# Kernel optimization log

Measured on AMD Instinct MI355X. Metric: run time of the kernel, lower is better.

## Reference

```python
import jax, jax.numpy as jnp
from jax import lax
import numpy as np

B, A, F, S, NA = 16, 5, 4, 45, 6


def _xavier(key, shape, fan_in, fan_out):
    lim = float(np.sqrt(6.0 / (fan_in + fan_out)))
    return jax.random.uniform(key, shape, jnp.float32, -lim, lim)


def setup_inputs() -> dict:
    key = jax.random.key(0)
    ks = jax.random.split(key, 16)
    x = jax.random.uniform(ks[0], (B, A, F, S, S, S), jnp.float32, 0.0, 255.0)
    p = lambda: jnp.full((1,), 0.25, jnp.float32)  # PReLU init
    return {
        "x": x,
        "conv0_w": _xavier(ks[1], (32, F, 5, 5, 5), F * 125, 32 * 125),
        "conv0_b": jnp.zeros((32,), jnp.float32),
        "prelu0": p(),
        "conv1_w": _xavier(ks[2], (32, 32, 5, 5, 5), 32 * 125, 32 * 125),
        "conv1_b": jnp.zeros((32,), jnp.float32),
        "prelu1": p(),
        "conv2_w": _xavier(ks[3], (64, 32, 4, 4, 4), 32 * 64, 64 * 64),
        "conv2_b": jnp.zeros((64,), jnp.float32),
        "prelu2": p(),
        "conv3_w": _xavier(ks[4], (64, 64, 3, 3, 3), 64 * 27, 64 * 27),
        "conv3_b": jnp.zeros((64,), jnp.float32),
        "prelu3": p(),
        "fc1_w": _xavier(ks[5], (A, 256, 1024), 1024, 256),
        "fc1_b": jnp.zeros((A, 256), jnp.float32),
        "prelu4": p(),
        "fc2_w": _xavier(ks[6], (A, 128, 512), 512, 128),
        "fc2_b": jnp.zeros((A, 128), jnp.float32),
        "prelu5": p(),
        "fc3_w": _xavier(ks[7], (A, NA, 256), 256, NA),
        "fc3_b": jnp.zeros((A, NA), jnp.float32),
    }


def _conv3d(x, w, b, pad):
    y = lax.conv_general_dilated(
        x, w, window_strides=(1, 1, 1), padding=[(pad, pad)] * 3,
        dimension_numbers=("NCDHW", "OIDHW", "NCDHW"))
    return y + b[None, :, None, None, None]


def _maxpool2(x):
    return lax.reduce_window(x, -jnp.inf, lax.max,
                             (1, 1, 2, 2, 2), (1, 1, 2, 2, 2), "VALID")


def _prelu(x, a):
    return jnp.where(x >= 0, x, a * x)


def _comm_fc(feat, w, b):
    # feat: [B,A,D]; w: [A,O,2D]; b: [A,O]. concat(feat, mean-over-agents) -> per-agent linear
    comm = jnp.mean(feat, axis=1, keepdims=True)
    cat = jnp.concatenate([feat, jnp.broadcast_to(comm, feat.shape)], axis=-1)
    return jnp.einsum("bai,aoi->bao", cat, w) + b[None]


def reference(x, conv0_w, conv0_b, prelu0, conv1_w, conv1_b, prelu1,
              conv2_w, conv2_b, prelu2, conv3_w, conv3_b, prelu3,
              fc1_w, fc1_b, prelu4, fc2_w, fc2_b, prelu5, fc3_w, fc3_b):
    b, a = x.shape[0], x.shape[1]
    # fold agents into batch: conv stack is shared across agents
    h = x.reshape((b * a,) + x.shape[2:]) / 255.0
    h = _maxpool2(_prelu(_conv3d(h, conv0_w, conv0_b, 1), prelu0))
    h = _maxpool2(_prelu(_conv3d(h, conv1_w, conv1_b, 1), prelu1))
    h = _maxpool2(_prelu(_conv3d(h, conv2_w, conv2_b, 1), prelu2))
    h = _prelu(_conv3d(h, conv3_w, conv3_b, 0), prelu3)
    feat = h.reshape(b, a, -1)  # [B, A, 512]
    feat = _prelu(_comm_fc(feat, fc1_w, fc1_b), prelu4)   # [B, A, 256]
    feat = _prelu(_comm_fc(feat, fc2_w, fc2_b), prelu5)   # [B, A, 128]
    return _comm_fc(feat, fc3_w, fc3_b)                   # [B, A, NA]
```

## Files before the change

### kernel.cpp

```cpp
#include <hip/hip_runtime.h>


typedef __attribute__((ext_vector_type(8)))  _Float16 f16x8;
typedef __attribute__((ext_vector_type(8), aligned(8))) _Float16 f16x8u;
typedef __attribute__((ext_vector_type(4)))  float f32x4;

__device__ __forceinline__ ushort f2h(float f) {
    union { _Float16 h; ushort u; } v;
    v.h = (_Float16)f;
    return v.u;
}
__device__ __forceinline__ float h2f(ushort h) {
    union { ushort u; _Float16 h; } v; v.u = h;
    return (float)v.h;
}

#define MFMA16(A, B, C) __builtin_amdgcn_mfma_f32_16x16x32_f16(A, B, C, 0, 0, 0)

__global__ void pad_input_kernel(const float* __restrict__ x,
                                 ushort* __restrict__ hi)
{
    int t = blockIdx.x * 256 + threadIdx.x;
    const int TOT = 80 * 45 * 45 * 45;
    if (t >= TOT) return;
    int xi = t % 45, r = t / 45;
    int y = r % 45; r /= 45;
    int z = r % 45; int n = r / 45;
    int ib = ((n * 4) * 91125) + z * 2025 + y * 45 + xi;
    int ob = (((n * 47 + z + 1) * 47 + y + 1) * 48 + xi + 1) * 4;
    ushort h4[4];
    #pragma unroll
    for (int ic = 0; ic < 4; ++ic) {
        float v = x[ib + ic * 91125] * (1.f / 255.f);
        h4[ic] = f2h(v);
    }
    *(ushort4*)(hi + ob) = *(ushort4*)h4;
}

__global__ void pack_w0(const float* __restrict__ w, ushort* __restrict__ Bp,
                        int4* __restrict__ Dt)
{
    int t = blockIdx.x * 256 + threadIdx.x;
    if (t < 19 * 2 * 64 * 8) {
        int j = t & 7, l = (t >> 3) & 63, ot = (t >> 9) & 1, s = t >> 10;
        int oc = ot * 16 + (l & 15);
        int k = 32 * s + ((l >> 4) << 3) + j;
        float v = 0.f;
        if (k < 600) {
            int ic = k & 3, t6 = k >> 2;
            int kx = t6 % 6, q = t6 / 6, ky = q % 5, kz = q / 5;
            if (kx < 5) v = w[(oc * 4 + ic) * 125 + kz * 25 + ky * 5 + kx];
        }
        Bp[t] = f2h(v);
    }
    if (t < 19) {
        int dd[4];
        #pragma unroll
        for (int q = 0; q < 4; ++q) {
            int k = 32 * t + 8 * q;
            if (k < 600) {
                int t6 = k >> 2;
                int kx = t6 % 6, qq = t6 / 6;
                dd[q] = (((qq / 5) * 47 + (qq % 5)) * 48 + kx) * 4;
            } else dd[q] = 0;
        }
        int4 d; d.x = dd[0]; d.y = dd[1]; d.z = dd[2]; d.w = dd[3];
        Dt[t] = d;
    }
}

__global__ void pack_w1(const float* __restrict__ w, ushort* __restrict__ Bp,
                        int* __restrict__ Dt)
{
    int t = blockIdx.x * 256 + threadIdx.x;
    if (t < 126 * 2 * 64 * 8) {
        int j = t & 7, l = (t >> 3) & 63, ot = (t >> 9) & 1, s = t >> 10;
        int oc = ot * 16 + (l & 15);
        int ic = ((l >> 4) << 3) + j;
        Bp[t] = (s < 125) ? f2h(w[(oc * 32 + ic) * 125 + s]) : (ushort)0;
    }
    if (t < 126) {
        if (t < 125) {
            int kz = t / 25, ky = (t / 5) % 5, kx = t % 5;
            Dt[t] = ((kz * 23 + ky) * 24 + kx) * 32;
        } else Dt[t] = 0;
    }
}

__global__ void pack_w2(const float* __restrict__ w,
                        ushort* __restrict__ Bh, ushort* __restrict__ Bl,
                        int* __restrict__ Dt)
{
    int t = blockIdx.x * 256 + threadIdx.x;
    if (t < 64 * 4 * 64 * 8) {
        int j = t & 7, l = (t >> 3) & 63, nt = (t >> 9) & 3, s = t >> 11;
        int oc = nt * 16 + (l & 15);
        int ic = ((l >> 4) << 3) + j;
        int kz = s >> 4, ky = (s >> 2) & 3, kx = s & 3;
        float v = w[(oc * 32 + ic) * 64 + kz * 16 + ky * 4 + kx];
        ushort h = f2h(v);
        Bh[t] = h;
        Bl[t] = f2h(v - h2f(h));
    }
    if (t < 64) {
        int kz = t >> 4, ky = (t >> 2) & 3, kx = t & 3;
        Dt[t] = ((kz * 11 + ky) * 12 + kx) * 32;
    }
}

__global__ __launch_bounds__(256, 2)
void conv0_mfma(const ushort* __restrict__ hi0,
                const ushort* __restrict__ Bp, const int4* __restrict__ Dt,
                const float* __restrict__ bias, const float* __restrict__ slope,
                ushort* __restrict__ hi1)
{
    const int n   = blockIdx.z;
    const int pz  = blockIdx.x / 11, pyg = blockIdx.x % 11;
    const int tid = threadIdx.x, lane = tid & 63, w = tid >> 6;
    const int dz  = w >> 1, pyl = w & 1;
    const int py  = 2 * pyg + pyl;
    const int l15 = lane & 15, q = lane >> 4;

    __shared__ float pool[2][2][21][32];
    __shared__ __align__(16) ushort Bl[19 * 2 * 64 * 8];

    {
        const uint4* src = (const uint4*)Bp;
        uint4* dst = (uint4*)Bl;
        for (int i = tid; i < 2432; i += 256) dst[i] = src[i];
    }

    const int z0 = 2 * pz + dz;
    const int y0 = 2 * py;
    const float sl = slope[0];

    int ab[3];
    #pragma unroll
    for (int xt = 0; xt < 3; ++xt) {
        int x = xt * 16 + l15;
        int xr = x > 41 ? 41 : x;
        ab[xt] = (((n * 47 + z0) * 47 + y0) * 48 + xr) * 4;
    }

    f32x4 acc[2][3][2] = {};
    const f16x8* BL = (const f16x8*)Bl;

    f16x8 avd[2][3][2];

    auto LOADS = [&](int s, int j) {
        int4 dd = Dt[s];
        int delta = q == 0 ? dd.x : q == 1 ? dd.y : q == 2 ? dd.z : dd.w;
        #pragma unroll
        for (int xt = 0; xt < 3; ++xt) {
            int vo = ab[xt] + delta;
            avd[j][xt][0] = *(const f16x8u*)(hi0 + vo);
            avd[j][xt][1] = *(const f16x8u*)(hi0 + vo + 192);
        }
    };
    auto COMP = [&](int s, int j) {
        f16x8 b0 = BL[(2 * s) * 64 + lane];
        f16x8 b1 = BL[(2 * s + 1) * 64 + lane];
        #pragma unroll
        for (int xt = 0; xt < 3; ++xt)
            #pragma unroll
            for (int dy = 0; dy < 2; ++dy) {
                acc[dy][xt][0] = MFMA16(avd[j][xt][dy], b0, acc[dy][xt][0]);
                acc[dy][xt][1] = MFMA16(avd[j][xt][dy], b1, acc[dy][xt][1]);
            }
    };

    __syncthreads();

    LOADS(0, 0); LOADS(1, 1);
    for (int s = 0; s < 16; s += 2) {
        COMP(s, 0);     LOADS(s + 2, 0);
        COMP(s + 1, 1); LOADS(s + 3, 1);
    }
    COMP(16, 0); LOADS(18, 0);
    COMP(17, 1);
    COMP(18, 0);

    #pragma unroll
    for (int xt = 0; xt < 3; ++xt)
        #pragma unroll
        for (int ot = 0; ot < 2; ++ot) {
            float m0 = fmaxf(acc[0][xt][ot][0], acc[1][xt][ot][0]);
            float m1 = fmaxf(acc[0][xt][ot][1], acc[1][xt][ot][1]);
            float m2 = fmaxf(acc[0][xt][ot][2], acc[1][xt][ot][2]);
            float m3 = fmaxf(acc[0][xt][ot][3], acc[1][xt][ot][3]);
            int pxe = xt * 8 + 2 * q, pxo = pxe + 1;
            if (pxe < 21) pool[dz][pyl][pxe][ot * 16 + l15] = fmaxf(m0, m1);
            if (pxo < 21) pool[dz][pyl][pxo][ot * 16 + l15] = fmaxf(m2, m3);
        }
    __syncthreads();

    for (int t2 = tid; t2 < 1344; t2 += 256) {
        int oc = t2 & 31, r = t2 >> 5;
        int px = r % 21, pyl2 = r / 21;
        int py2 = 2 * pyg + pyl2;
        if (py2 > 20) continue;
        float v = fmaxf(pool[0][pyl2][px][oc], pool[1][pyl2][px][oc]);
        v += bias[oc];
        v = (v >= 0.f) ? v : sl * v;
        int o = (((n * 23 + pz + 1) * 23 + py2 + 1) * 24 + px + 1) * 32 + oc;
        hi1[o] = f2h(v);
    }
}

__global__ __launch_bounds__(256)
void conv1_mfma(const ushort* __restrict__ hi1,
                const ushort* __restrict__ Bp, const int* __restrict__ Dt,
                const float* __restrict__ bias, const float* __restrict__ slope,
                ushort* __restrict__ P2h, ushort* __restrict__ P2l)
{
    const int n   = blockIdx.z;
    const int pz  = blockIdx.x / 3, pyg = blockIdx.x % 3;
    const int tid = threadIdx.x, lane = tid & 63, w = tid >> 6;
    const int dz = w >> 1, dy = w & 1;
    const int q = lane >> 4, l15 = lane & 15;

    __shared__ float pool[4][27][32];
    const int z0 = 2 * pz + dz;

    int ab[4];
    #pragma unroll
    for (int t = 0; t < 4; ++t) {
        int flat = t * 16 + l15;
        if (flat > 53) flat = 53;
        int pyl = flat / 18, x = flat - pyl * 18;
        int y0 = 2 * (pyg * 3 + pyl) + dy;
        ab[t] = ((((n * 23 + z0) * 23 + y0) * 24 + x) << 5) + q * 8;
    }

    f32x4 acc[4][2] = {};
    const f16x8* Bv = (const f16x8*)Bp;

    f16x8 ahv[3][4], b0v[3], b1v[3];

    auto LOADS = [&](int s, int j) {
        int off = Dt[s];
        b0v[j] = Bv[(2 * s) * 64 + lane];
        b1v[j] = Bv[(2 * s + 1) * 64 + lane];
        #pragma unroll
        for (int t = 0; t < 4; ++t)
            ahv[j][t] = *(const f16x8*)(hi1 + ab[t] + off);
    };
    auto COMP = [&](int j) {
        #pragma unroll
        for (int t = 0; t < 4; ++t) {
            acc[t][0] = MFMA16(ahv[j][t], b0v[j], acc[t][0]);
            acc[t][1] = MFMA16(ahv[j][t], b1v[j], acc[t][1]);
        }
    };

    LOADS(0, 0); LOADS(1, 1);
    for (int s = 0; s < 123; s += 3) {
        LOADS(s + 2, 2); COMP(0);
        LOADS(s + 3, 0); COMP(1);
        LOADS(s + 4, 1); COMP(2);
    }
    LOADS(125, 2);
    COMP(0); COMP(1); COMP(2);

    #pragma unroll
    for (int t = 0; t < 4; ++t) {
        int p0 = t * 8 + q * 2;
        float e0 = fmaxf(acc[t][0][0], acc[t][0][1]);
        float o0 = fmaxf(acc[t][0][2], acc[t][0][3]);
        float e1 = fmaxf(acc[t][1][0], acc[t][1][1]);
        float o1 = fmaxf(acc[t][1][2], acc[t][1][3]);
        if (p0 < 27)     { pool[w][p0][l15] = e0;     pool[w][p0][16 + l15] = e1; }
        if (p0 + 1 < 27) { pool[w][p0 + 1][l15] = o0; pool[w][p0 + 1][16 + l15] = o1; }
    }
    __syncthreads();

    for (int t2 = tid; t2 < 864; t2 += 256) {
        int oc = t2 & 31, pr = t2 >> 5;
        int pyl = pr / 9, px = pr % 9;
        float v = fmaxf(fmaxf(pool[0][pr][oc], pool[1][pr][oc]),
                        fmaxf(pool[2][pr][oc], pool[3][pr][oc]));
        v += bias[oc];
        float s0 = slope[0];
        v = (v >= 0.f) ? v : s0 * v;
        int py = pyg * 3 + pyl;
        int o = (((n * 11 + pz + 1) * 11 + py + 1) * 12 + px + 1) * 32 + oc;
        ushort h = f2h(v);
        P2h[o] = h;
        P2l[o] = f2h(v - h2f(h));
    }
}

__global__ __launch_bounds__(256)
void conv2_mfma(const ushort* __restrict__ P2h, const ushort* __restrict__ P2l,
                const ushort* __restrict__ Bph, const ushort* __restrict__ Bpl,
                const int* __restrict__ Dt,
                const float* __restrict__ bias, const float* __restrict__ slope,
                float* __restrict__ P3)
{
    const int n  = blockIdx.x >> 2, zq = blockIdx.x & 3;
    const int tid = threadIdx.x, lane = tid & 63, w = tid >> 6;
    const int q = lane >> 4, l15 = lane & 15;

    __shared__ float pool[2][2][4][4][64];

    const int ozl = w >> 1, oyp0 = 2 * (w & 1);
    const int oz  = zq * 2 + ozl;
    const int myA = l15 >> 3, mxA = l15 & 7;

    int ab[2];
    ab[0] = (((n * 11 + oz) * 11 + oyp0 * 2 + myA) * 12 + mxA) * 32 + q * 8;
    ab[1] = ab[0] + 2 * 12 * 32;

    f32x4 acc[2][4] = {};
    const f16x8* BH = (const f16x8*)Bph;
    const f16x8* BL = (const f16x8*)Bpl;

    f16x8 ahv[2][2], alv[2][2], bhv[2][4], blv[2][4];

    auto LOADS = [&](int s, int j) {
        int d = Dt[s];
        #pragma unroll
        for (int t = 0; t < 2; ++t) {
            ahv[j][t] = *(const f16x8u*)(P2h + ab[t] + d);
            alv[j][t] = *(const f16x8u*)(P2l + ab[t] + d);
        }
        #pragma unroll
        for (int nt = 0; nt < 4; ++nt) {
            bhv[j][nt] = BH[(s * 4 + nt) * 64 + lane];
            blv[j][nt] = BL[(s * 4 + nt) * 64 + lane];
        }
    };
    auto COMP = [&](int j) {
        #pragma unroll
        for (int t = 0; t < 2; ++t)
            #pragma unroll
            for (int nt = 0; nt < 4; ++nt) {
                acc[t][nt] = MFMA16(ahv[j][t], bhv[j][nt], acc[t][nt]);
                acc[t][nt] = MFMA16(alv[j][t], bhv[j][nt], acc[t][nt]);
                acc[t][nt] = MFMA16(ahv[j][t], blv[j][nt], acc[t][nt]);
            }
    };

    LOADS(0, 0); LOADS(1, 1);
    for (int s = 0; s < 62; s += 2) {
        COMP(0); LOADS(s + 2, 0);
        COMP(1); LOADS(s + 3, 1);
    }
    COMP(0); COMP(1);

    const int myD = q >> 1, pxe = (q & 1) * 2;
    #pragma unroll
    for (int t = 0; t < 2; ++t) {
        int py = oyp0 + t;
        #pragma unroll
        for (int nt = 0; nt < 4; ++nt) {
            int oc = nt * 16 + l15;
            pool[myD][ozl][py][pxe][oc]     = fmaxf(acc[t][nt][0], acc[t][nt][1]);
            pool[myD][ozl][py][pxe + 1][oc] = fmaxf(acc[t][nt][2], acc[t][nt][3]);
        }
    }
    __syncthreads();

    for (int t2 = tid; t2 < 1024; t2 += 256) {
        int oc = t2 & 63, r = t2 >> 6;
        int py = r >> 2, px = r & 3;
        float v = fmaxf(fmaxf(pool[0][0][py][px][oc], pool[0][1][py][px][oc]),
                        fmaxf(pool[1][0][py][px][oc], pool[1][1][py][px][oc]));
        v += bias[oc];
        float a = slope[0];
        v = (v >= 0.f) ? v : a * v;
        P3[((long)n * 64 + oc) * 64 + zq * 16 + py * 4 + px] = v;
    }
}

__global__ void conv3_kernel(const float* __restrict__ in,
                             const float* __restrict__ w,
                             const float* __restrict__ bias,
                             const float* __restrict__ slope,
                             float* __restrict__ out)
{
    int idx = blockIdx.x * blockDim.x + threadIdx.x;
    const int TOTAL = 80 * 64 * 8;
    if (idx >= TOTAL) return;
    int p  = idx & 7;
    int oc = (idx >> 3) & 63;
    int n  = idx >> 9;
    int ox = p & 1, oy = (p >> 1) & 1, oz = p >> 2;

    const float* inb = in + (long)n * 64 * 64;
    const float* wb  = w + (long)oc * 64 * 27;

    float acc = 0.f;
    for (int ic = 0; ic < 64; ++ic) {
        const float* inc = inb + ic * 64;
        const float* wc  = wb + ic * 27;
        #pragma unroll
        for (int kz = 0; kz < 3; ++kz)
            #pragma unroll
            for (int ky = 0; ky < 3; ++ky)
                #pragma unroll
                for (int kx = 0; kx < 3; ++kx)
                    acc += wc[(kz * 3 + ky) * 3 + kx] *
                           inc[((oz + kz) * 4 + (oy + ky)) * 4 + (ox + kx)];
    }
    float v = acc + bias[oc];
    float a = slope[0];
    v = (v >= 0.f) ? v : a * v;
    out[idx] = v;
}

template<int D, int O, bool PRELU_ON>
__global__ void comm_fc_kernel(const float* __restrict__ feat,
                               const float* __restrict__ w,
                               const float* __restrict__ bias,
                               const float* __restrict__ slope,
                               float* __restrict__ out)
{
    const int a = blockIdx.x;
    const int b = blockIdx.y;

    __shared__ __align__(16) float cat[2 * D];
    for (int i = threadIdx.x; i < D; i += blockDim.x) {
        float m = 0.f;
        #pragma unroll
        for (int aa = 0; aa < 5; ++aa) m += feat[(b * 5 + aa) * D + i];
        cat[i]     = feat[(b * 5 + a) * D + i];
        cat[D + i] = m * 0.2f;
    }
    __syncthreads();

    for (int o = threadIdx.x; o < O; o += blockDim.x) {
        const float4* wr = (const float4*)(w + ((long)(a * O) + o) * 2 * D);
        const float4* cr = (const float4*)cat;
        float acc = 0.f;
        for (int i = 0; i < 2 * D / 4; ++i) {
            float4 wv = wr[i];
            float4 cv = cr[i];
            acc += wv.x * cv.x + wv.y * cv.y + wv.z * cv.z + wv.w * cv.w;
        }
        acc += bias[a * O + o];
        if constexpr (PRELU_ON) {
            float s = slope[0];
            acc = (acc >= 0.f) ? acc : s * acc;
        }
        out[(b * 5 + a) * O + o] = acc;
    }
}

extern "C" void kernel_launch(void* const* d_in, const int* in_sizes, int n_in,
                              void* d_out, int out_size, void* d_ws, size_t ws_size,
                              hipStream_t stream)
{
    const float* x    = (const float*)d_in[0];
    const float* c0w  = (const float*)d_in[1];
    const float* c0b  = (const float*)d_in[2];
    const float* p0   = (const float*)d_in[3];
    const float* c1w  = (const float*)d_in[4];
    const float* c1b  = (const float*)d_in[5];
    const float* p1   = (const float*)d_in[6];
    const float* c2w  = (const float*)d_in[7];
    const float* c2b  = (const float*)d_in[8];
    const float* p2   = (const float*)d_in[9];
    const float* c3w  = (const float*)d_in[10];
    const float* c3b  = (const float*)d_in[11];
    const float* p3   = (const float*)d_in[12];
    const float* f1w  = (const float*)d_in[13];
    const float* f1b  = (const float*)d_in[14];
    const float* p4   = (const float*)d_in[15];
    const float* f2w  = (const float*)d_in[16];
    const float* f2b  = (const float*)d_in[17];
    const float* p5   = (const float*)d_in[18];
    const float* f3w  = (const float*)d_in[19];
    const float* f3b  = (const float*)d_in[20];

    char* ws = (char*)d_ws;
    ushort* hi0  = (ushort*)(ws);
    ushort* hi1  = (ushort*)(ws + 67860480);
    ushort* P2h  = (ushort*)(ws + 132864000);
    ushort* P2l  = (ushort*)(ws + 140298240);
    float*  P3   = (float*) (ws + 147732480);
    float*  feat0= (float*) (ws + 149043200);
    float*  feat1= (float*) (ws + 149207040);
    float*  feat2= (float*) (ws + 149288960);
    ushort* Bp0  = (ushort*)(ws + 149329920);
    ushort* Bp1  = (ushort*)(ws + 149368832);
    int4*   Dt0  = (int4*)  (ws + 149626880);
    int*    Dt1  = (int*)   (ws + 149627184);
    ushort* Bp2h = (ushort*)(ws + 149700000);
    ushort* Bp2l = (ushort*)(ws + 149962144);
    int*    Dt2  = (int*)   (ws + 150224288);

    hipMemsetAsync(ws, 0, 147732480, stream);

    pack_w0<<<76, 256, 0, stream>>>(c0w, Bp0, Dt0);
    pack_w1<<<504, 256, 0, stream>>>(c1w, Bp1, Dt1);
    pack_w2<<<512, 256, 0, stream>>>(c2w, Bp2h, Bp2l, Dt2);
    pad_input_kernel<<<(7290000 + 255) / 256, 256, 0, stream>>>(x, hi0);

    conv0_mfma<<<dim3(231, 1, 80), 256, 0, stream>>>(hi0, Bp0, Dt0,
                                                     c0b, p0, hi1);
    conv1_mfma<<<dim3(27, 1, 80), 256, 0, stream>>>(hi1, Bp1, Dt1,
                                                    c1b, p1, P2h, P2l);
    conv2_mfma<<<dim3(320), 256, 0, stream>>>(P2h, P2l, Bp2h, Bp2l, Dt2,
                                              c2b, p2, P3);

    conv3_kernel<<<dim3(160), dim3(256), 0, stream>>>(P3, c3w, c3b, p3, feat0);

    comm_fc_kernel<512, 256, true>
        <<<dim3(5, 16), dim3(256), 0, stream>>>(feat0, f1w, f1b, p4, feat1);
    comm_fc_kernel<256, 128, true>
        <<<dim3(5, 16), dim3(256), 0, stream>>>(feat1, f2w, f2b, p5, feat2);
    comm_fc_kernel<128, 6, false>
        <<<dim3(5, 16), dim3(64), 0, stream>>>(feat2, f3w, f3b, nullptr, (float*)d_out);
}
```

Measured before the change: 1.022 ms.

## Stage conv0/conv1 input tiles in LDS and write padding in pad kernel

conv0 now copies the padded input slab for its block into shared memory and reads A fragments from LDS, while weights are read from global memory instead of LDS. conv1 streams z-planes of its input through a three-slot LDS ring buffer with register staging, replacing per-tap global loads. The pad kernel now writes the zero halo itself, so the workspace memset skips the hi0 region. The aim is to cut redundant global and L2 traffic from overlapping conv windows, at the cost of extra LDS use, lower occupancy and more barriers.

New measurement: 862.0 us. 1.19x faster.

```diff
diff --git a/kernel.cpp b/kernel.cpp
--- a/kernel.cpp
+++ b/kernel.cpp
@@ -21,24 +21,23 @@
                                  ushort* __restrict__ hi)
 {
     int t = blockIdx.x * 256 + threadIdx.x;
-    const int TOT = 80 * 45 * 45 * 45;
+    const int TOT = 80 * 47 * 47 * 48;
     if (t >= TOT) return;
-    int xi = t % 45, r = t / 45;
-    int y = r % 45; r /= 45;
-    int z = r % 45; int n = r / 45;
-    int ib = ((n * 4) * 91125) + z * 2025 + y * 45 + xi;
-    int ob = (((n * 47 + z + 1) * 47 + y + 1) * 48 + xi + 1) * 4;
-    ushort h4[4];
-    #pragma unroll
-    for (int ic = 0; ic < 4; ++ic) {
-        float v = x[ib + ic * 91125] * (1.f / 255.f);
-        h4[ic] = f2h(v);
-    }
-    *(ushort4*)(hi + ob) = *(ushort4*)h4;
+    int xo = t % 48, r = t / 48;
+    int yo = r % 47; r /= 47;
+    int zo = r % 47; int n = r / 47;
+    ushort h4[4] = {0, 0, 0, 0};
+    if (zo >= 1 && zo <= 45 && yo >= 1 && yo <= 45 && xo >= 1 && xo <= 45) {
+        int ib = n * 4 * 91125 + (zo - 1) * 2025 + (yo - 1) * 45 + (xo - 1);
+        #pragma unroll
+        for (int ic = 0; ic < 4; ++ic)
+            h4[ic] = f2h(x[ib + ic * 91125] * (1.f / 255.f));
+    }
+    *(ushort4*)(hi + t * 4) = *(ushort4*)h4;
 }
 
 __global__ void pack_w0(const float* __restrict__ w, ushort* __restrict__ Bp,
-                        int4* __restrict__ Dt)
+                        int4* __restrict__ DtL)
 {
     int t = blockIdx.x * 256 + threadIdx.x;
     if (t < 19 * 2 * 64 * 8) {
@@ -61,16 +60,15 @@
             if (k < 600) {
                 int t6 = k >> 2;
                 int kx = t6 % 6, qq = t6 / 6;
-                dd[q] = (((qq / 5) * 47 + (qq % 5)) * 48 + kx) * 4;
+                dd[q] = ((qq / 5) * 8 + (qq % 5)) * 192 + kx * 4;
             } else dd[q] = 0;
         }
         int4 d; d.x = dd[0]; d.y = dd[1]; d.z = dd[2]; d.w = dd[3];
-        Dt[t] = d;
-    }
-}
-
-__global__ void pack_w1(const float* __restrict__ w, ushort* __restrict__ Bp,
-                        int* __restrict__ Dt)
+        DtL[t] = d;
+    }
+}
+
+__global__ void pack_w1(const float* __restrict__ w, ushort* __restrict__ Bp)
 {
     int t = blockIdx.x * 256 + threadIdx.x;
     if (t < 126 * 2 * 64 * 8) {
@@ -78,12 +76,6 @@
         int oc = ot * 16 + (l & 15);
         int ic = ((l >> 4) << 3) + j;
         Bp[t] = (s < 125) ? f2h(w[(oc * 32 + ic) * 125 + s]) : (ushort)0;
-    }
-    if (t < 126) {
-        if (t < 125) {
-            int kz = t / 25, ky = (t / 5) % 5, kx = t % 5;
-            Dt[t] = ((kz * 23 + ky) * 24 + kx) * 32;
-        } else Dt[t] = 0;
     }
 }
 
@@ -108,9 +100,9 @@
     }
 }
 
-__global__ __launch_bounds__(256, 2)
+__global__ __launch_bounds__(256)
 void conv0_mfma(const ushort* __restrict__ hi0,
-                const ushort* __restrict__ Bp, const int4* __restrict__ Dt,
+                const ushort* __restrict__ Bp, const int4* __restrict__ DtL,
                 const float* __restrict__ bias, const float* __restrict__ slope,
                 ushort* __restrict__ hi1)
 {
@@ -118,54 +110,52 @@
     const int pz  = blockIdx.x / 11, pyg = blockIdx.x % 11;
     const int tid = threadIdx.x, lane = tid & 63, w = tid >> 6;
     const int dz  = w >> 1, pyl = w & 1;
-    const int py  = 2 * pyg + pyl;
     const int l15 = lane & 15, q = lane >> 4;
 
     __shared__ float pool[2][2][21][32];
-    __shared__ __align__(16) ushort Bl[19 * 2 * 64 * 8];
+    __shared__ __align__(16) ushort As[6 * 8 * 192];
 
     {
-        const uint4* src = (const uint4*)Bp;
-        uint4* dst = (uint4*)Bl;
-        for (int i = tid; i < 2432; i += 256) dst[i] = src[i];
-    }
-
-    const int z0 = 2 * pz + dz;
-    const int y0 = 2 * py;
+        const int base = ((n * 47 + 2 * pz) * 47 + 4 * pyg) * 192;
+        for (int u = tid; u < 2304; u += 256) {
+            int zr = u / 384, rem = u - zr * 384;
+            int src = base + zr * 9024 + rem * 4;
+            *(uint2*)(As + u * 4) = *(const uint2*)(hi0 + src);
+        }
+    }
+
     const float sl = slope[0];
-
-    int ab[3];
+    int lb[3];
     #pragma unroll
     for (int xt = 0; xt < 3; ++xt) {
         int x = xt * 16 + l15;
         int xr = x > 41 ? 41 : x;
-        ab[xt] = (((n * 47 + z0) * 47 + y0) * 48 + xr) * 4;
+        lb[xt] = (dz * 8 + 2 * pyl) * 192 + xr * 4;
     }
 
     f32x4 acc[2][3][2] = {};
-    const f16x8* BL = (const f16x8*)Bl;
-
-    f16x8 avd[2][3][2];
+    const f16x8* Bv = (const f16x8*)Bp;
+    f16x8 avd[2][3][2], b0v[2], b1v[2];
 
     auto LOADS = [&](int s, int j) {
-        int4 dd = Dt[s];
+        int4 dd = DtL[s];
         int delta = q == 0 ? dd.x : q == 1 ? dd.y : q == 2 ? dd.z : dd.w;
+        b0v[j] = Bv[(2 * s) * 64 + lane];
+        b1v[j] = Bv[(2 * s + 1) * 64 + lane];
         #pragma unroll
         for (int xt = 0; xt < 3; ++xt) {
-            int vo = ab[xt] + delta;
-            avd[j][xt][0] = *(const f16x8u*)(hi0 + vo);
-            avd[j][xt][1] = *(const f16x8u*)(hi0 + vo + 192);
+            const ushort* p = As + lb[xt] + delta;
+            avd[j][xt][0] = *(const f16x8u*)p;
+            avd[j][xt][1] = *(const f16x8u*)(p + 192);
         }
     };
-    auto COMP = [&](int s, int j) {
-        f16x8 b0 = BL[(2 * s) * 64 + lane];
-        f16x8 b1 = BL[(2 * s + 1) * 64 + lane];
+    auto COMP = [&](int j) {
         #pragma unroll
         for (int xt = 0; xt < 3; ++xt)
             #pragma unroll
             for (int dy = 0; dy < 2; ++dy) {
-                acc[dy][xt][0] = MFMA16(avd[j][xt][dy], b0, acc[dy][xt][0]);
-                acc[dy][xt][1] = MFMA16(avd[j][xt][dy], b1, acc[dy][xt][1]);
+                acc[dy][xt][0] = MFMA16(avd[j][xt][dy], b0v[j], acc[dy][xt][0]);
+                acc[dy][xt][1] = MFMA16(avd[j][xt][dy], b1v[j], acc[dy][xt][1]);
             }
     };
 
@@ -173,12 +163,12 @@
 
     LOADS(0, 0); LOADS(1, 1);
     for (int s = 0; s < 16; s += 2) {
-        COMP(s, 0);     LOADS(s + 2, 0);
-        COMP(s + 1, 1); LOADS(s + 3, 1);
-    }
-    COMP(16, 0); LOADS(18, 0);
-    COMP(17, 1);
-    COMP(18, 0);
+        COMP(0); LOADS(s + 2, 0);
+        COMP(1); LOADS(s + 3, 1);
+    }
+    COMP(0); LOADS(18, 0);
+    COMP(1);
+    COMP(0);
 
     #pragma unroll
     for (int xt = 0; xt < 3; ++xt)
@@ -209,7 +199,7 @@
 
 __global__ __launch_bounds__(256)
 void conv1_mfma(const ushort* __restrict__ hi1,
-                const ushort* __restrict__ Bp, const int* __restrict__ Dt,
+                const ushort* __restrict__ Bp,
                 const float* __restrict__ bias, const float* __restrict__ slope,
                 ushort* __restrict__ P2h, ushort* __restrict__ P2l)
 {
@@ -220,47 +210,76 @@
     const int q = lane >> 4, l15 = lane & 15;
 
     __shared__ float pool[4][27][32];
-    const int z0 = 2 * pz + dz;
-
-    int ab[4];
+    __shared__ __align__(16) ushort As[3 * 7680];
+
+    int lb[4];
     #pragma unroll
     for (int t = 0; t < 4; ++t) {
         int flat = t * 16 + l15;
         if (flat > 53) flat = 53;
         int pyl = flat / 18, x = flat - pyl * 18;
-        int y0 = 2 * (pyg * 3 + pyl) + dy;
-        ab[t] = ((((n * 23 + z0) * 23 + y0) * 24 + x) << 5) + q * 8;
-    }
+        lb[t] = (2 * pyl + dy) * 768 + x * 32 + q * 8;
+    }
+
+    f16x8 stg[4];
+    auto STAGE_LOAD = [&](int zoff) {
+        const ushort* src = hi1 + ((n * 23 + 2 * pz + zoff) * 23 + 6 * pyg) * 768;
+        #pragma unroll
+        for (int r = 0; r < 4; ++r) {
+            int u = tid + r * 256;
+            if (u < 960) stg[r] = *(const f16x8*)(src + u * 8);
+        }
+    };
+    auto STAGE_WRITE = [&](int zoff) {
+        int slot = zoff % 3;
+        #pragma unroll
+        for (int r = 0; r < 4; ++r) {
+            int u = tid + r * 256;
+            if (u < 960) *(f16x8*)(As + slot * 7680 + u * 8) = stg[r];
+        }
+    };
 
     f32x4 acc[4][2] = {};
     const f16x8* Bv = (const f16x8*)Bp;
-
-    f16x8 ahv[3][4], b0v[3], b1v[3];
-
-    auto LOADS = [&](int s, int j) {
-        int off = Dt[s];
-        b0v[j] = Bv[(2 * s) * 64 + lane];
-        b1v[j] = Bv[(2 * s + 1) * 64 + lane];
-        #pragma unroll
-        for (int t = 0; t < 4; ++t)
-            ahv[j][t] = *(const f16x8*)(hi1 + ab[t] + off);
-    };
-    auto COMP = [&](int j) {
-        #pragma unroll
-        for (int t = 0; t < 4; ++t) {
-            acc[t][0] = MFMA16(ahv[j][t], b0v[j], acc[t][0]);
-            acc[t][1] = MFMA16(ahv[j][t], b1v[j], acc[t][1]);
-        }
-    };
-
-    LOADS(0, 0); LOADS(1, 1);
-    for (int s = 0; s < 123; s += 3) {
-        LOADS(s + 2, 2); COMP(0);
-        LOADS(s + 3, 0); COMP(1);
-        LOADS(s + 4, 1); COMP(2);
-    }
-    LOADS(125, 2);
-    COMP(0); COMP(1); COMP(2);
+    f16x8 ahv[2][4], b0v[2], b1v[2];
+
+    STAGE_LOAD(0); STAGE_WRITE(0);
+    STAGE_LOAD(1); STAGE_WRITE(1);
+    __syncthreads();
+
+    for (int kz = 0; kz < 5; ++kz) {
+        if (kz < 4) STAGE_LOAD(kz + 2);
+        const int slotbase = ((dz + kz) % 3) * 7680;
+        const int sg0 = kz * 25;
+
+        auto LOADS = [&](int s, int j) {
+            int delta = (s / 5) * 768 + (s % 5) * 32;
+            int sg = sg0 + s;
+            b0v[j] = Bv[(2 * sg) * 64 + lane];
+            b1v[j] = Bv[(2 * sg + 1) * 64 + lane];
+            #pragma unroll
+            for (int t = 0; t < 4; ++t)
+                ahv[j][t] = *(const f16x8u*)(As + slotbase + lb[t] + delta);
+        };
+        auto COMP = [&](int j) {
+            #pragma unroll
+            for (int t = 0; t < 4; ++t) {
+                acc[t][0] = MFMA16(ahv[j][t], b0v[j], acc[t][0]);
+                acc[t][1] = MFMA16(ahv[j][t], b1v[j], acc[t][1]);
+            }
+        };
+
+        LOADS(0, 0); LOADS(1, 1);
+        for (int s = 0; s < 24; s += 2) {
+            COMP(0); LOADS(s + 2 > 24 ? 24 : s + 2, 0);
+            COMP(1); LOADS(s + 3 > 24 ? 24 : s + 3, 1);
+        }
+        COMP(0);
+
+        __syncthreads();
+        if (kz < 4) STAGE_WRITE(kz + 2);
+        __syncthreads();
+    }
 
     #pragma unroll
     for (int t = 0; t < 4; ++t) {
@@ -485,21 +504,20 @@
     ushort* Bp0  = (ushort*)(ws + 149329920);
     ushort* Bp1  = (ushort*)(ws + 149368832);
     int4*   Dt0  = (int4*)  (ws + 149626880);
-    int*    Dt1  = (int*)   (ws + 149627184);
     ushort* Bp2h = (ushort*)(ws + 149700000);
     ushort* Bp2l = (ushort*)(ws + 149962144);
     int*    Dt2  = (int*)   (ws + 150224288);
 
-    hipMemsetAsync(ws, 0, 147732480, stream);
+    hipMemsetAsync(ws + 67860480, 0, 79872000, stream);
 
     pack_w0<<<76, 256, 0, stream>>>(c0w, Bp0, Dt0);
-    pack_w1<<<504, 256, 0, stream>>>(c1w, Bp1, Dt1);
+    pack_w1<<<504, 256, 0, stream>>>(c1w, Bp1);
     pack_w2<<<512, 256, 0, stream>>>(c2w, Bp2h, Bp2l, Dt2);
-    pad_input_kernel<<<(7290000 + 255) / 256, 256, 0, stream>>>(x, hi0);
+    pad_input_kernel<<<(80 * 47 * 47 * 48 + 255) / 256, 256, 0, stream>>>(x, hi0);
 
     conv0_mfma<<<dim3(231, 1, 80), 256, 0, stream>>>(hi0, Bp0, Dt0,
                                                      c0b, p0, hi1);
-    conv1_mfma<<<dim3(27, 1, 80), 256, 0, stream>>>(hi1, Bp1, Dt1,
+    conv1_mfma<<<dim3(27, 1, 80), 256, 0, stream>>>(hi1, Bp1,
                                                     c1b, p1, P2h, P2l);
     conv2_mfma<<<dim3(320), 256, 0, stream>>>(P2h, P2l, Bp2h, Bp2l, Dt2,
                                               c2b, p2, P3);
```
